# Optimization experiments

Hardware: AMD Instinct MI355X
Metric: run time of the kernel (lower is better)

The kernel has to match this reference:

```python
import jax, jax.numpy as jnp
import numpy as np

EPS = 1e-8
SIM_THRESHOLD = 0.5


def _conv(x, src, dst, W, b):
    # Gather per-edge endpoint features: x_j = source, x_i = target (PyG default flow)
    x_j = x[src]
    x_i = x[dst]
    # Cosine similarity per edge
    dot = jnp.sum(x_i * x_j, axis=1)
    denom = jnp.maximum(jnp.linalg.norm(x_i, axis=1) * jnp.linalg.norm(x_j, axis=1), EPS)
    sim = dot / denom
    mask = (sim > SIM_THRESHOLD).astype(x.dtype)[:, None]
    msg = x_j * mask
    # Scatter-add aggregate into target nodes
    agg = jax.ops.segment_sum(msg, dst, num_segments=x.shape[0])
    # update: Linear
    return agg @ W.T + b


def setup_inputs() -> dict:
    key = jax.random.key(0)
    k1, k2, k3, k4, k5 = jax.random.split(key, 5)
    N, E, D_IN, D_HID, D_OUT = 50000, 800000, 128, 256, 64
    x = jax.random.normal(k1, (N, D_IN), dtype=jnp.float32)
    edge_index = jax.random.randint(k2, (2, E), 0, N, dtype=jnp.int64)
    # Xavier-uniform linear weights, zero-ish bias
    lim1 = float(np.sqrt(6.0 / (D_IN + D_HID)))
    lim2 = float(np.sqrt(6.0 / (D_HID + D_OUT)))
    W1 = jax.random.uniform(k3, (D_HID, D_IN), minval=-lim1, maxval=lim1, dtype=jnp.float32)
    b1 = jnp.zeros((D_HID,), dtype=jnp.float32)
    W2 = jax.random.uniform(k4, (D_OUT, D_HID), minval=-lim2, maxval=lim2, dtype=jnp.float32)
    b2 = jnp.zeros((D_OUT,), dtype=jnp.float32)
    return {"x": x, "edge_index": edge_index, "W1": W1, "b1": b1, "W2": W2, "b2": b2}


def reference(x, edge_index, W1, b1, W2, b2):
    N = x.shape[0]
    # add self-loops
    loops = jnp.arange(N, dtype=edge_index.dtype)
    src = jnp.concatenate([edge_index[0], loops])
    dst = jnp.concatenate([edge_index[1], loops])
    h = _conv(x, src, dst, W1, b1)
    h = jax.nn.relu(h)  # dropout is identity in eval mode
    out = _conv(h, src, dst, W2, b2)
    return jax.nn.log_softmax(out, axis=-1)
```

## Files before the change

kernel.cpp:

```cpp
#include <hip/hip_runtime.h>
#include <math.h>

#define EPS 1e-8f
#define NB_SORT 256

#if defined(__has_builtin)
#if __has_builtin(__builtin_amdgcn_sdot4)
#define HAVE_SDOT4 1
#endif
#endif

typedef __attribute__((ext_vector_type(8))) short bf16x8;
typedef __attribute__((ext_vector_type(4))) float f32x4;

__device__ __forceinline__ int sdot4i(int a, int b, int c) {
#ifdef HAVE_SDOT4
  return __builtin_amdgcn_sdot4(a, b, c, false);
#else
  return c + ((int)(signed char)(a)) * ((int)(signed char)(b)) +
         ((int)(signed char)(a >> 8)) * ((int)(signed char)(b >> 8)) +
         ((int)(signed char)(a >> 16)) * ((int)(signed char)(b >> 16)) +
         (a >> 24) * (b >> 24);
#endif
}

__device__ __forceinline__ float wave_reduce_sum(float v) {
#pragma unroll
  for (int off = 32; off > 0; off >>= 1)
    v += __shfl_xor(v, off, 64);
  return v;
}

__device__ __forceinline__ float wave_reduce_max(float v) {
#pragma unroll
  for (int off = 32; off > 0; off >>= 1)
    v = fmaxf(v, __shfl_xor(v, off, 64));
  return v;
}

__device__ __forceinline__ float dot4(float4 a, float4 b) {
  return a.x * b.x + a.y * b.y + a.z * b.z + a.w * b.w;
}

__device__ __forceinline__ int clampq(float q) {
  int i = (int)rintf(q);
  return i < -127 ? -127 : (i > 127 ? 127 : i);
}

__device__ __forceinline__ void split_bf16(float x, unsigned int& hi,
                                           unsigned int& lo) {
  unsigned int u = __float_as_uint(x);
  hi = u >> 16;
  float hf = __uint_as_float(u & 0xFFFF0000u);
  float r = x - hf;
  lo = __float_as_uint(r) >> 16;
}

__global__ __launch_bounds__(256) void hist_coarse(const int* __restrict__ dst,
                                                   int* __restrict__ hist_blk,
                                                   int E, int nbuck) {
  __shared__ int lh[1024];
  int t = threadIdx.x, blk = blockIdx.x;
  for (int i = t; i < nbuck; i += 256) lh[i] = 0;
  __syncthreads();
  int ch = (E + NB_SORT - 1) / NB_SORT;
  int lo = blk * ch, hi = min(E, lo + ch);
  for (int e = lo + t; e < hi; e += 256) atomicAdd(&lh[dst[e] >> 6], 1);
  __syncthreads();
  for (int i = t; i < nbuck; i += 256) hist_blk[i * NB_SORT + blk] = lh[i];
}

__global__ __launch_bounds__(256) void scan_local(int* __restrict__ hist,
                                                  int* __restrict__ bsum,
                                                  int nb) {
  __shared__ int tsum[256];
  int t = threadIdx.x;
  int base = blockIdx.x * 1024 + t * 4;
  int v0 = 0, v1 = 0, v2 = 0, v3 = 0;
  if (base + 3 < nb) {
    int4 q = *(const int4*)&hist[base];
    v0 = q.x; v1 = q.y; v2 = q.z; v3 = q.w;
  } else {
    if (base + 0 < nb) v0 = hist[base + 0];
    if (base + 1 < nb) v1 = hist[base + 1];
    if (base + 2 < nb) v2 = hist[base + 2];
  }
  tsum[t] = v0 + v1 + v2 + v3;
  __syncthreads();
  for (int off = 1; off < 256; off <<= 1) {
    int u = 0;
    if (t >= off) u = tsum[t - off];
    __syncthreads();
    if (t >= off) tsum[t] += u;
    __syncthreads();
  }
  int excl = (t == 0) ? 0 : tsum[t - 1];
  int e0 = excl, e1 = excl + v0, e2 = e1 + v1, e3 = e2 + v2;
  if (base + 3 < nb) {
    *(int4*)&hist[base] = make_int4(e0, e1, e2, e3);
  } else {
    if (base + 0 < nb) hist[base + 0] = e0;
    if (base + 1 < nb) hist[base + 1] = e1;
    if (base + 2 < nb) hist[base + 2] = e2;
  }
  if (t == 255) bsum[blockIdx.x] = tsum[255];
}

__global__ __launch_bounds__(256) void scan_bsum(int* __restrict__ bsum,
                                                 int nblk) {
  __shared__ int sh[256];
  int t = threadIdx.x;
  sh[t] = (t < nblk) ? bsum[t] : 0;
  __syncthreads();
  for (int off = 1; off < 256; off <<= 1) {
    int u = 0;
    if (t >= off) u = sh[t - off];
    __syncthreads();
    if (t >= off) sh[t] += u;
    __syncthreads();
  }
  if (t < nblk) bsum[t] = (t == 0) ? 0 : sh[t - 1];
}

__global__ __launch_bounds__(256) void add_bsum(int* __restrict__ hist,
                                                const int* __restrict__ bsum,
                                                int nb) {
  int i = blockIdx.x * blockDim.x + threadIdx.x;
  if (i < nb) hist[i] += bsum[i >> 10];
}

__global__ __launch_bounds__(256) void scatter_coarse(
    const int* __restrict__ src, const int* __restrict__ dst,
    const int* __restrict__ S, int2* __restrict__ epair, int E, int nbuck) {
  __shared__ int lb[1024];
  int t = threadIdx.x, blk = blockIdx.x;
  for (int i = t; i < nbuck; i += 256) lb[i] = S[i * NB_SORT + blk];
  __syncthreads();
  int ch = (E + NB_SORT - 1) / NB_SORT;
  int lo = blk * ch, hi = min(E, lo + ch);
  for (int e = lo + t; e < hi; e += 256) {
    int d = dst[e];
    int pos = atomicAdd(&lb[d >> 6], 1);
    epair[pos] = make_int2(src[e], d);
  }
}

__global__ __launch_bounds__(256) void fine_sort(
    const int2* __restrict__ epair, const int* __restrict__ S,
    int* __restrict__ ssrc, int* __restrict__ endoff, int E, int nbuck,
    int N) {
  __shared__ int fh[64];
  __shared__ int cur[64];
  int b = blockIdx.x, t = threadIdx.x;
  int bstart = S[b * NB_SORT];
  int bend = (b + 1 < nbuck) ? S[(b + 1) * NB_SORT] : E;
  if (t < 64) fh[t] = 0;
  __syncthreads();
  for (int e = bstart + t; e < bend; e += 256)
    atomicAdd(&fh[epair[e].y & 63], 1);
  __syncthreads();
  if (t < 64) {
    int v = fh[t];
    int incl = v;
#pragma unroll
    for (int off = 1; off < 64; off <<= 1) {
      int u = __shfl_up(incl, off, 64);
      if (t >= off) incl += u;
    }
    cur[t] = incl - v;
    int d = b * 64 + t;
    if (d < N) endoff[d] = bstart + incl;
  }
  __syncthreads();
  for (int e = bstart + t; e < bend; e += 256) {
    int2 p = epair[e];
    int pos = atomicAdd(&cur[p.y & 63], 1);
    ssrc[bstart + pos] = p.x;
  }
}

__global__ __launch_bounds__(256) void prep_x(const float* __restrict__ x,
                                              signed char* __restrict__ qx,
                                              float4* __restrict__ nprop,
                                              float* __restrict__ agg,
                                              int N) {
  int node = (int)((blockIdx.x * blockDim.x + threadIdx.x) >> 6);
  int lane = threadIdx.x & 63;
  if (node >= N) return;
  float2 v = *(const float2*)(x + (size_t)node * 128 + lane * 2);
  float ax = fabsf(v.x), ay = fabsf(v.y);
  float mx = wave_reduce_max(fmaxf(ax, ay));
  float l1 = wave_reduce_sum(ax + ay);
  float ss = wave_reduce_sum(v.x * v.x + v.y * v.y);
  float s = mx * (1.0f / 127.0f);
  float inv = (mx > 0.f) ? 127.0f / mx : 0.f;
  int q0 = clampq(v.x * inv), q1 = clampq(v.y * inv);
  unsigned short w = (unsigned short)((q0 & 0xff) | ((q1 & 0xff) << 8));
  ((unsigned short*)(qx + (size_t)node * 128))[lane] = w;
  float l1q = s * wave_reduce_sum((float)(abs(q0) + abs(q1)));
  bool sp = ss > 0.5f * fmaxf(ss, EPS);
  *(float2*)(agg + (size_t)node * 128 + lane * 2) =
      sp ? v : make_float2(0.f, 0.f);
  if (lane == 0)
    nprop[node] = make_float4(sqrtf(ss), s, fmaxf(l1, l1q), 0.f);
}

__global__ __launch_bounds__(256) void prep_h(const float* __restrict__ h,
                                              signed char* __restrict__ qh,
                                              float4* __restrict__ nprop,
                                              float* __restrict__ agg,
                                              int N) {
  int node = (int)((blockIdx.x * blockDim.x + threadIdx.x) >> 6);
  int lane = threadIdx.x & 63;
  if (node >= N) return;
  float4 v = *(const float4*)(h + (size_t)node * 256 + lane * 4);
  float ax = fabsf(v.x), ay = fabsf(v.y), az = fabsf(v.z), aw = fabsf(v.w);
  float mx = wave_reduce_max(fmaxf(fmaxf(ax, ay), fmaxf(az, aw)));
  float l1 = wave_reduce_sum(ax + ay + az + aw);
  float ss = wave_reduce_sum(dot4(v, v));
  float s = mx * (1.0f / 127.0f);
  float inv = (mx > 0.f) ? 127.0f / mx : 0.f;
  int q0 = clampq(v.x * inv), q1 = clampq(v.y * inv);
  int q2 = clampq(v.z * inv), q3 = clampq(v.w * inv);
  int w = (q0 & 0xff) | ((q1 & 0xff) << 8) | ((q2 & 0xff) << 16) | (q3 << 24);
  ((int*)(qh + (size_t)node * 256))[lane] = w;
  float l1q = s * wave_reduce_sum((float)(abs(q0) + abs(q1) + abs(q2) + abs(q3)));
  bool sp = ss > 0.5f * fmaxf(ss, EPS);
  *(float4*)(agg + (size_t)node * 256 + lane * 4) =
      sp ? v : make_float4(0.f, 0.f, 0.f, 0.f);
  if (lane == 0)
    nprop[node] = make_float4(sqrtf(ss), s, fmaxf(l1, l1q), 0.f);
}

template <int D>
__global__ __launch_bounds__(512) void conv_lpe(
    const float* __restrict__ xf, const signed char* __restrict__ qt,
    const float4* __restrict__ nprop, const int* __restrict__ ssrc,
    const int* __restrict__ endoff, float* __restrict__ agg, int N) {
  constexpr int RB = D + 16;
  constexpr int NG = D / 16;
  constexpr int V = D / 64;
  __shared__ signed char qtile[64 * RB];
  __shared__ float4 npd[64];
  __shared__ int eoff[65];
  const int tid = threadIdx.x;
  const int lane = tid & 63;
  const int n0 = blockIdx.x * 64;

  if (tid < 65) {
    int idx = n0 - 1 + tid;
    eoff[tid] = (idx < 0) ? 0 : endoff[min(idx, N - 1)];
  }
  if (tid >= 64 && tid < 128) {
    int i = tid - 64;
    int n = n0 + i;
    npd[i] = (n < N) ? nprop[n] : make_float4(0.f, 0.f, 0.f, 0.f);
  }
  for (int j = tid; j < 64 * NG; j += 512) {
    int r = j / NG, c = j % NG;
    int n = n0 + r;
    int4 v = (n < N) ? *(const int4*)(qt + (size_t)n * D + c * 16)
                     : make_int4(0, 0, 0, 0);
    *(int4*)(qtile + r * RB + c * 16) = v;
  }
  __syncthreads();

  const int bstart = eoff[0];
  const int bend = eoff[64];

  for (int base = bstart; base < bend; base += 512) {
    int e0 = base + tid;
    bool valid = e0 < bend;
    int s = valid ? ssrc[e0] : 0;
    float4 nps = valid ? nprop[s] : make_float4(0.f, 0.f, 0.f, 0.f);
    int lo = 0, hi = 63;
#pragma unroll
    for (int it = 0; it < 6; ++it) {
      int mid = (lo + hi) >> 1;
      if (e0 >= eoff[mid + 1]) lo = mid + 1; else hi = mid;
    }
    const int dloc = lo;
    float4 npdl = npd[dloc];
    const signed char* srow = qt + (size_t)s * D;
    const signed char* drow = qtile + dloc * RB;
    int id = 0;
#pragma unroll
    for (int g = 0; g < NG; ++g) {
      int4 a = *(const int4*)(srow + g * 16);
      int4 bq = *(const int4*)(drow + g * 16);
      id = sdot4i(a.x, bq.x, id);
      id = sdot4i(a.y, bq.y, id);
      id = sdot4i(a.z, bq.z, id);
      id = sdot4i(a.w, bq.w, id);
    }
    float denom = fmaxf(nps.x * npdl.x, EPS);
    float thr = 0.5f * denom;
    float approx = (nps.y * npdl.y) * (float)id;
    float m = 0.5002f * (nps.y * npdl.z + npdl.y * nps.z) + 2e-6f * denom + 1e-7f;
    bool maybe = valid && (approx > thr - m);
    unsigned long long mask = __ballot(maybe);
    while (mask) {
      int ln = __ffsll((long long)mask) - 1;
      mask &= mask - 1;
      int es = __shfl(s, ln);
      int dl = __shfl(dloc, ln);
      float nsx = __shfl(nps.x, ln);
      int dn = n0 + dl;
      float sv[V], dvv[V];
      if constexpr (V == 2) {
        float2 a = *(const float2*)(xf + (size_t)es * D + lane * 2);
        float2 b = *(const float2*)(xf + (size_t)dn * D + lane * 2);
        sv[0] = a.x; sv[1] = a.y; dvv[0] = b.x; dvv[1] = b.y;
      } else {
        float4 a = *(const float4*)(xf + (size_t)es * D + lane * 4);
        float4 b = *(const float4*)(xf + (size_t)dn * D + lane * 4);
        sv[0] = a.x; sv[1] = a.y; sv[2] = a.z; sv[3] = a.w;
        dvv[0] = b.x; dvv[1] = b.y; dvv[2] = b.z; dvv[3] = b.w;
      }
      float dx = 0.f;
#pragma unroll
      for (int q = 0; q < V; ++q) dx += sv[q] * dvv[q];
      dx = wave_reduce_sum(dx);
      float ndx = npd[dl].x;
      if (dx > 0.5f * fmaxf(nsx * ndx, EPS)) {
        float* arow = agg + (size_t)dn * D + lane * V;
#pragma unroll
        for (int q = 0; q < V; ++q) atomicAdd(&arow[q], sv[q]);
      }
    }
  }
}

__global__ __launch_bounds__(256) void gemm1_mfma(
    const float* __restrict__ A, const float* __restrict__ W,
    const float* __restrict__ bias, float* __restrict__ C, int M) {
  constexpr int K = 128, NN = 256, BM = 128, BK = 32, PK = 40;
  __shared__ unsigned short Ah[BM * PK];
  __shared__ unsigned short Al[BM * PK];
  __shared__ unsigned short Wh[BM * PK];
  __shared__ unsigned short Wl[BM * PK];
  const int tid = threadIdx.x;
  const int m0 = blockIdx.x * BM;
  const int n0 = blockIdx.y * BM;
  const int lane = tid & 63;
  const int wv = tid >> 6;
  const int wr = wv >> 1, wc = wv & 1;
  const int lrow = lane & 15, kg = lane >> 4;
  f32x4 acc[4][4] = {};

  for (int k0 = 0; k0 < K; k0 += BK) {
#pragma unroll
    for (int i = 0; i < 4; ++i) {
      int f = tid + i * 256;
      int r = f >> 3, q = f & 7;
      int gm = m0 + r;
      float4 a = (gm < M) ? *(const float4*)&A[(size_t)gm * K + k0 + q * 4]
                          : make_float4(0.f, 0.f, 0.f, 0.f);
      float4 w = *(const float4*)&W[(size_t)(n0 + r) * K + k0 + q * 4];
      unsigned int h0, h1, h2, h3, l0, l1, l2, l3;
      split_bf16(a.x, h0, l0); split_bf16(a.y, h1, l1);
      split_bf16(a.z, h2, l2); split_bf16(a.w, h3, l3);
      *(uint2*)&Ah[r * PK + q * 4] =
          make_uint2(h0 | (h1 << 16), h2 | (h3 << 16));
      *(uint2*)&Al[r * PK + q * 4] =
          make_uint2(l0 | (l1 << 16), l2 | (l3 << 16));
      split_bf16(w.x, h0, l0); split_bf16(w.y, h1, l1);
      split_bf16(w.z, h2, l2); split_bf16(w.w, h3, l3);
      *(uint2*)&Wh[r * PK + q * 4] =
          make_uint2(h0 | (h1 << 16), h2 | (h3 << 16));
      *(uint2*)&Wl[r * PK + q * 4] =
          make_uint2(l0 | (l1 << 16), l2 | (l3 << 16));
    }
    __syncthreads();
    bf16x8 ah[4], al[4], bh[4], bl[4];
#pragma unroll
    for (int m = 0; m < 4; ++m) {
      int row = wr * 64 + m * 16 + lrow;
      ah[m] = *(const bf16x8*)&Ah[row * PK + kg * 8];
      al[m] = *(const bf16x8*)&Al[row * PK + kg * 8];
    }
#pragma unroll
    for (int n = 0; n < 4; ++n) {
      int row = wc * 64 + n * 16 + lrow;
      bh[n] = *(const bf16x8*)&Wh[row * PK + kg * 8];
      bl[n] = *(const bf16x8*)&Wl[row * PK + kg * 8];
    }
#pragma unroll
    for (int m = 0; m < 4; ++m)
#pragma unroll
      for (int n = 0; n < 4; ++n) {
        acc[m][n] = __builtin_amdgcn_mfma_f32_16x16x32_bf16(ah[m], bh[n],
                                                            acc[m][n], 0, 0, 0);
        acc[m][n] = __builtin_amdgcn_mfma_f32_16x16x32_bf16(ah[m], bl[n],
                                                            acc[m][n], 0, 0, 0);
        acc[m][n] = __builtin_amdgcn_mfma_f32_16x16x32_bf16(al[m], bh[n],
                                                            acc[m][n], 0, 0, 0);
      }
    __syncthreads();
  }

#pragma unroll
  for (int n = 0; n < 4; ++n) {
    int gc = n0 + wc * 64 + n * 16 + lrow;
    float bv = bias[gc];
#pragma unroll
    for (int m = 0; m < 4; ++m) {
      int gr0 = m0 + wr * 64 + m * 16 + kg * 4;
#pragma unroll
      for (int r = 0; r < 4; ++r) {
        int gm = gr0 + r;
        if (gm < M) {
          float v = acc[m][n][r] + bv;
          C[(size_t)gm * NN + gc] = fmaxf(v, 0.f);
        }
      }
    }
  }
}

__global__ __launch_bounds__(256) void split_w2(
    const float* __restrict__ W, unsigned short* __restrict__ Wh,
    unsigned short* __restrict__ Wl, int total4) {
  int i = blockIdx.x * 256 + threadIdx.x;
  if (i >= total4) return;
  float4 w = ((const float4*)W)[i];
  unsigned int h0, h1, h2, h3, l0, l1, l2, l3;
  split_bf16(w.x, h0, l0); split_bf16(w.y, h1, l1);
  split_bf16(w.z, h2, l2); split_bf16(w.w, h3, l3);
  ((uint2*)Wh)[i] = make_uint2(h0 | (h1 << 16), h2 | (h3 << 16));
  ((uint2*)Wl)[i] = make_uint2(l0 | (l1 << 16), l2 | (l3 << 16));
}

__global__ __launch_bounds__(256) void gemm2_mfma_lsm(
    const float* __restrict__ A, const unsigned short* __restrict__ Wh,
    const unsigned short* __restrict__ Wl, const float* __restrict__ bias,
    float* __restrict__ out, int M) {
  constexpr int K = 256;
  const int tid = threadIdx.x;
  const int lane = tid & 63;
  const int wv = tid >> 6;
  const int lrow = lane & 15, kg = lane >> 4;
  const int r0 = blockIdx.x * 128 + wv * 32;
  f32x4 acc[2][4] = {};

  for (int k0 = 0; k0 < K; k0 += 32) {
    bf16x8 ah[2], al[2];
#pragma unroll
    for (int m = 0; m < 2; ++m) {
      int row = r0 + m * 16 + lrow;
      const float* ap = A + (size_t)row * K + k0 + kg * 8;
      float4 a0 = *(const float4*)ap;
      float4 a1 = *(const float4*)(ap + 4);
      unsigned int hh[8], ll[8];
      split_bf16(a0.x, hh[0], ll[0]); split_bf16(a0.y, hh[1], ll[1]);
      split_bf16(a0.z, hh[2], ll[2]); split_bf16(a0.w, hh[3], ll[3]);
      split_bf16(a1.x, hh[4], ll[4]); split_bf16(a1.y, hh[5], ll[5]);
      split_bf16(a1.z, hh[6], ll[6]); split_bf16(a1.w, hh[7], ll[7]);
      bf16x8 th, tl;
#pragma unroll
      for (int j = 0; j < 8; ++j) {
        th[j] = (short)hh[j];
        tl[j] = (short)ll[j];
      }
      ah[m] = th;
      al[m] = tl;
    }
    bf16x8 bh[4], bl[4];
#pragma unroll
    for (int n = 0; n < 4; ++n) {
      int wrow = n * 16 + lrow;
      bh[n] = *(const bf16x8*)&Wh[(size_t)wrow * K + k0 + kg * 8];
      bl[n] = *(const bf16x8*)&Wl[(size_t)wrow * K + k0 + kg * 8];
    }
#pragma unroll
    for (int m = 0; m < 2; ++m)
#pragma unroll
      for (int n = 0; n < 4; ++n) {
        acc[m][n] = __builtin_amdgcn_mfma_f32_16x16x32_bf16(ah[m], bh[n],
                                                            acc[m][n], 0, 0, 0);
        acc[m][n] = __builtin_amdgcn_mfma_f32_16x16x32_bf16(ah[m], bl[n],
                                                            acc[m][n], 0, 0, 0);
        acc[m][n] = __builtin_amdgcn_mfma_f32_16x16x32_bf16(al[m], bh[n],
                                                            acc[m][n], 0, 0, 0);
      }
  }

  float bv[4];
#pragma unroll
  for (int n = 0; n < 4; ++n) bv[n] = bias[n * 16 + lrow];
#pragma unroll
  for (int m = 0; m < 2; ++m)
#pragma unroll
    for (int r = 0; r < 4; ++r) {
      int row = r0 + m * 16 + kg * 4 + r;
      float v[4];
      float mx = -1e30f;
#pragma unroll
      for (int n = 0; n < 4; ++n) {
        v[n] = acc[m][n][r] + bv[n];
        mx = fmaxf(mx, v[n]);
      }
#pragma unroll
      for (int off = 8; off > 0; off >>= 1)
        mx = fmaxf(mx, __shfl_xor(mx, off, 64));
      float s = 0.f;
#pragma unroll
      for (int n = 0; n < 4; ++n) s += expf(v[n] - mx);
#pragma unroll
      for (int off = 8; off > 0; off >>= 1) s += __shfl_xor(s, off, 64);
      float lg = logf(s);
      if (row < M) {
#pragma unroll
        for (int n = 0; n < 4; ++n)
          out[(size_t)row * 64 + n * 16 + lrow] = v[n] - mx - lg;
      }
    }
}

extern "C" void kernel_launch(void* const* d_in, const int* in_sizes, int n_in,
                              void* d_out, int out_size, void* d_ws,
                              size_t ws_size, hipStream_t stream) {
  const float* x  = (const float*)d_in[0];
  const int* eidx = (const int*)d_in[1];
  const float* W1 = (const float*)d_in[2];
  const float* b1 = (const float*)d_in[3];
  const float* W2 = (const float*)d_in[4];
  const float* b2 = (const float*)d_in[5];
  float* out = (float*)d_out;

  const int N = in_sizes[0] / 128;
  const int E = in_sizes[1] / 2;
  const int* src = eidx;
  const int* dst = eidx + E;

  const int nbuck = (N + 63) / 64;
  const int ntot = nbuck * NB_SORT;
  const int nblk2 = (ntot + 1023) / 1024;

  float* agg    = (float*)d_ws;
  float* h      = agg + (size_t)N * 256;
  float4* npx   = (float4*)(h + (size_t)N * 256);
  float4* nph   = npx + N;
  int* S        = (int*)(nph + N);
  int* bsum     = S + ntot;
  int* ssrc     = bsum + 256;
  int* endoff   = ssrc + E;
  signed char* qh = (signed char*)(endoff + N);
  unsigned short* W2h = (unsigned short*)(qh + (size_t)N * 256);
  unsigned short* W2l = W2h + 64 * 256;
  int2* epair   = (int2*)h;
  signed char* qx = (signed char*)(h + (size_t)N * 64);

  split_w2<<<16, 256, 0, stream>>>(W2, W2h, W2l, 64 * 256 / 4);

  hist_coarse<<<NB_SORT, 256, 0, stream>>>(dst, S, E, nbuck);
  scan_local<<<nblk2, 256, 0, stream>>>(S, bsum, ntot);
  scan_bsum<<<1, 256, 0, stream>>>(bsum, nblk2);
  add_bsum<<<(ntot + 255) / 256, 256, 0, stream>>>(S, bsum, ntot);
  scatter_coarse<<<NB_SORT, 256, 0, stream>>>(src, dst, S, epair, E, nbuck);
  fine_sort<<<nbuck, 256, 0, stream>>>(epair, S, ssrc, endoff, E, nbuck, N);

  prep_x<<<(N + 3) / 4, 256, 0, stream>>>(x, qx, npx, agg, N);
  conv_lpe<128><<<nbuck, 512, 0, stream>>>(x, qx, npx, ssrc, endoff, agg, N);
  gemm1_mfma<<<dim3((N + 127) / 128, 2), 256, 0, stream>>>(agg, W1, b1, h, N);

  prep_h<<<(N + 3) / 4, 256, 0, stream>>>(h, qh, nph, agg, N);
  conv_lpe<256><<<nbuck, 512, 0, stream>>>(h, qh, nph, ssrc, endoff, agg, N);
  gemm2_mfma_lsm<<<dim3((N + 127) / 128), 256, 0, stream>>>(agg, W2h, W2l, b2,
                                                            out, N);
}
```

Measured before the change: 300.6 us.

## Replace per-destination-tile conv with flat edge-parallel conv over sorted edge pairs

The sorting pass now emits (src,dst) pairs sorted by destination instead of a source array plus per-node end offsets. The convolution kernels become flat edge-parallel launches with one thread per edge, so the LDS-staged destination tile, the offset binary search and per-block load imbalance are dropped. The price is that destination quantized rows and node properties are read from global memory (or cache) for each edge, and the pair array takes twice the space of the source array.

```diff
diff --git a/kernel.cpp b/kernel.cpp
--- a/kernel.cpp
+++ b/kernel.cpp
@@ -147,8 +147,7 @@
 
 __global__ __launch_bounds__(256) void fine_sort(
     const int2* __restrict__ epair, const int* __restrict__ S,
-    int* __restrict__ ssrc, int* __restrict__ endoff, int E, int nbuck,
-    int N) {
+    int2* __restrict__ spair, int E, int nbuck) {
   __shared__ int fh[64];
   __shared__ int cur[64];
   int b = blockIdx.x, t = threadIdx.x;
@@ -168,14 +167,12 @@
       if (t >= off) incl += u;
     }
     cur[t] = incl - v;
-    int d = b * 64 + t;
-    if (d < N) endoff[d] = bstart + incl;
   }
   __syncthreads();
   for (int e = bstart + t; e < bend; e += 256) {
     int2 p = epair[e];
     int pos = atomicAdd(&cur[p.y & 63], 1);
-    ssrc[bstart + pos] = p.x;
+    spair[bstart + pos] = p;
   }
 }
 
@@ -233,100 +230,63 @@
 }
 
 template <int D>
-__global__ __launch_bounds__(512) void conv_lpe(
+__global__ __launch_bounds__(256) void conv_flat(
     const float* __restrict__ xf, const signed char* __restrict__ qt,
-    const float4* __restrict__ nprop, const int* __restrict__ ssrc,
-    const int* __restrict__ endoff, float* __restrict__ agg, int N) {
-  constexpr int RB = D + 16;
+    const float4* __restrict__ nprop, const int2* __restrict__ spair,
+    float* __restrict__ agg, int E) {
   constexpr int NG = D / 16;
   constexpr int V = D / 64;
-  __shared__ signed char qtile[64 * RB];
-  __shared__ float4 npd[64];
-  __shared__ int eoff[65];
-  const int tid = threadIdx.x;
-  const int lane = tid & 63;
-  const int n0 = blockIdx.x * 64;
-
-  if (tid < 65) {
-    int idx = n0 - 1 + tid;
-    eoff[tid] = (idx < 0) ? 0 : endoff[min(idx, N - 1)];
-  }
-  if (tid >= 64 && tid < 128) {
-    int i = tid - 64;
-    int n = n0 + i;
-    npd[i] = (n < N) ? nprop[n] : make_float4(0.f, 0.f, 0.f, 0.f);
-  }
-  for (int j = tid; j < 64 * NG; j += 512) {
-    int r = j / NG, c = j % NG;
-    int n = n0 + r;
-    int4 v = (n < N) ? *(const int4*)(qt + (size_t)n * D + c * 16)
-                     : make_int4(0, 0, 0, 0);
-    *(int4*)(qtile + r * RB + c * 16) = v;
-  }
-  __syncthreads();
-
-  const int bstart = eoff[0];
-  const int bend = eoff[64];
-
-  for (int base = bstart; base < bend; base += 512) {
-    int e0 = base + tid;
-    bool valid = e0 < bend;
-    int s = valid ? ssrc[e0] : 0;
-    float4 nps = valid ? nprop[s] : make_float4(0.f, 0.f, 0.f, 0.f);
-    int lo = 0, hi = 63;
-#pragma unroll
-    for (int it = 0; it < 6; ++it) {
-      int mid = (lo + hi) >> 1;
-      if (e0 >= eoff[mid + 1]) lo = mid + 1; else hi = mid;
-    }
-    const int dloc = lo;
-    float4 npdl = npd[dloc];
-    const signed char* srow = qt + (size_t)s * D;
-    const signed char* drow = qtile + dloc * RB;
-    int id = 0;
-#pragma unroll
-    for (int g = 0; g < NG; ++g) {
-      int4 a = *(const int4*)(srow + g * 16);
-      int4 bq = *(const int4*)(drow + g * 16);
-      id = sdot4i(a.x, bq.x, id);
-      id = sdot4i(a.y, bq.y, id);
-      id = sdot4i(a.z, bq.z, id);
-      id = sdot4i(a.w, bq.w, id);
-    }
-    float denom = fmaxf(nps.x * npdl.x, EPS);
-    float thr = 0.5f * denom;
-    float approx = (nps.y * npdl.y) * (float)id;
-    float m = 0.5002f * (nps.y * npdl.z + npdl.y * nps.z) + 2e-6f * denom + 1e-7f;
-    bool maybe = valid && (approx > thr - m);
-    unsigned long long mask = __ballot(maybe);
-    while (mask) {
-      int ln = __ffsll((long long)mask) - 1;
-      mask &= mask - 1;
-      int es = __shfl(s, ln);
-      int dl = __shfl(dloc, ln);
-      float nsx = __shfl(nps.x, ln);
-      int dn = n0 + dl;
-      float sv[V], dvv[V];
-      if constexpr (V == 2) {
-        float2 a = *(const float2*)(xf + (size_t)es * D + lane * 2);
-        float2 b = *(const float2*)(xf + (size_t)dn * D + lane * 2);
-        sv[0] = a.x; sv[1] = a.y; dvv[0] = b.x; dvv[1] = b.y;
-      } else {
-        float4 a = *(const float4*)(xf + (size_t)es * D + lane * 4);
-        float4 b = *(const float4*)(xf + (size_t)dn * D + lane * 4);
-        sv[0] = a.x; sv[1] = a.y; sv[2] = a.z; sv[3] = a.w;
-        dvv[0] = b.x; dvv[1] = b.y; dvv[2] = b.z; dvv[3] = b.w;
-      }
-      float dx = 0.f;
-#pragma unroll
-      for (int q = 0; q < V; ++q) dx += sv[q] * dvv[q];
-      dx = wave_reduce_sum(dx);
-      float ndx = npd[dl].x;
-      if (dx > 0.5f * fmaxf(nsx * ndx, EPS)) {
-        float* arow = agg + (size_t)dn * D + lane * V;
-#pragma unroll
-        for (int q = 0; q < V; ++q) atomicAdd(&arow[q], sv[q]);
-      }
+  const int e0 = blockIdx.x * 256 + threadIdx.x;
+  const int lane = threadIdx.x & 63;
+  const bool valid = e0 < E;
+  int2 p = valid ? spair[e0] : make_int2(0, 0);
+  const int s = p.x, d = p.y;
+  float4 nps = nprop[s];
+  float4 npd = nprop[d];
+  const signed char* srow = qt + (size_t)s * D;
+  const signed char* drow = qt + (size_t)d * D;
+  int id = 0;
+#pragma unroll
+  for (int g = 0; g < NG; ++g) {
+    int4 a = *(const int4*)(srow + g * 16);
+    int4 bq = *(const int4*)(drow + g * 16);
+    id = sdot4i(a.x, bq.x, id);
+    id = sdot4i(a.y, bq.y, id);
+    id = sdot4i(a.z, bq.z, id);
+    id = sdot4i(a.w, bq.w, id);
+  }
+  float denom = fmaxf(nps.x * npd.x, EPS);
+  float thr = 0.5f * denom;
+  float approx = (nps.y * npd.y) * (float)id;
+  float m = 0.5002f * (nps.y * npd.z + npd.y * nps.z) + 2e-6f * denom + 1e-7f;
+  bool maybe = valid && (approx > thr - m);
+  unsigned long long mask = __ballot(maybe);
+  while (mask) {
+    int ln = __ffsll((long long)mask) - 1;
+    mask &= mask - 1;
+    int es = __shfl(s, ln);
+    int ed = __shfl(d, ln);
+    float nsx = __shfl(nps.x, ln);
+    float ndx = __shfl(npd.x, ln);
+    float sv[V], dvv[V];
+    if constexpr (V == 2) {
+      float2 a = *(const float2*)(xf + (size_t)es * D + lane * 2);
+      float2 b = *(const float2*)(xf + (size_t)ed * D + lane * 2);
+      sv[0] = a.x; sv[1] = a.y; dvv[0] = b.x; dvv[1] = b.y;
+    } else {
+      float4 a = *(const float4*)(xf + (size_t)es * D + lane * 4);
+      float4 b = *(const float4*)(xf + (size_t)ed * D + lane * 4);
+      sv[0] = a.x; sv[1] = a.y; sv[2] = a.z; sv[3] = a.w;
+      dvv[0] = b.x; dvv[1] = b.y; dvv[2] = b.z; dvv[3] = b.w;
+    }
+    float dx = 0.f;
+#pragma unroll
+    for (int q = 0; q < V; ++q) dx += sv[q] * dvv[q];
+    dx = wave_reduce_sum(dx);
+    if (dx > 0.5f * fmaxf(nsx * ndx, EPS)) {
+      float* arow = agg + (size_t)ed * D + lane * V;
+#pragma unroll
+      for (int q = 0; q < V; ++q) atomicAdd(&arow[q], sv[q]);
     }
   }
 }
@@ -543,9 +503,8 @@
   float4* nph   = npx + N;
   int* S        = (int*)(nph + N);
   int* bsum     = S + ntot;
-  int* ssrc     = bsum + 256;
-  int* endoff   = ssrc + E;
-  signed char* qh = (signed char*)(endoff + N);
+  int2* spair   = (int2*)(bsum + 256);
+  signed char* qh = (signed char*)(spair + E);
   unsigned short* W2h = (unsigned short*)(qh + (size_t)N * 256);
   unsigned short* W2l = W2h + 64 * 256;
   int2* epair   = (int2*)h;
@@ -558,14 +517,16 @@
   scan_bsum<<<1, 256, 0, stream>>>(bsum, nblk2);
   add_bsum<<<(ntot + 255) / 256, 256, 0, stream>>>(S, bsum, ntot);
   scatter_coarse<<<NB_SORT, 256, 0, stream>>>(src, dst, S, epair, E, nbuck);
-  fine_sort<<<nbuck, 256, 0, stream>>>(epair, S, ssrc, endoff, E, nbuck, N);
+  fine_sort<<<nbuck, 256, 0, stream>>>(epair, S, spair, E, nbuck);
+
+  const int nblkE = (E + 255) / 256;
 
   prep_x<<<(N + 3) / 4, 256, 0, stream>>>(x, qx, npx, agg, N);
-  conv_lpe<128><<<nbuck, 512, 0, stream>>>(x, qx, npx, ssrc, endoff, agg, N);
+  conv_flat<128><<<nblkE, 256, 0, stream>>>(x, qx, npx, spair, agg, E);
   gemm1_mfma<<<dim3((N + 127) / 128, 2), 256, 0, stream>>>(agg, W1, b1, h, N);
 
   prep_h<<<(N + 3) / 4, 256, 0, stream>>>(h, qh, nph, agg, N);
-  conv_lpe<256><<<nbuck, 512, 0, stream>>>(h, qh, nph, ssrc, endoff, agg, N);
+  conv_flat<256><<<nblkE, 256, 0, stream>>>(h, qh, nph, spair, agg, E);
   gemm2_mfma_lsm<<<dim3((N + 127) / 128), 256, 0, stream>>>(agg, W2h, W2l, b2,
                                                             out, N);
 }
```

Measured after the change: 296.2 us. About the same (-1.5%).
